# Kernel optimization log

Hardware: AMD Instinct MI355X
Metric: run time of the kernel (lower is better)

The kernel has to match this reference:

```python
import jax, jax.numpy as jnp
import numpy as np

N_NODES = 100000
N_EDGES = 1600000
EMB = 64       # embedding_dim
HID = 128      # hidden_channels
N_GRAPHS = 512
N_TASKS = 128
ATOM_VOCAB = 119
BOND_VOCAB = 16


def setup_inputs() -> dict:
    key = jax.random.key(0)
    ks = jax.random.split(key, 24)
    s = 0.02
    inp = {
        'x_idx': jax.random.randint(ks[0], (N_NODES,), 0, ATOM_VOCAB),
        'edge_index': jax.random.randint(ks[1], (2, N_EDGES), 0, N_NODES),
        'edge_attr_idx': jax.random.randint(ks[2], (N_EDGES,), 0, BOND_VOCAB),
        'batch': jnp.sort(jax.random.randint(ks[3], (N_NODES,), 0, N_GRAPHS)),
        'atom_emb': jax.random.normal(ks[4], (ATOM_VOCAB, EMB), jnp.float32) * s,
        'bond_emb': jax.random.normal(ks[5], (BOND_VOCAB, EMB), jnp.float32) * s,
        'w_edge0': jax.random.normal(ks[6], (EMB, EMB), jnp.float32) * s,
        'b_edge0': jnp.zeros((EMB,), jnp.float32),
        'w1_0': jax.random.normal(ks[7], (EMB, HID), jnp.float32) * s,
        'b1_0': jnp.zeros((HID,), jnp.float32),
        'w2_0': jax.random.normal(ks[8], (HID, HID), jnp.float32) * s,
        'b2_0': jnp.zeros((HID,), jnp.float32),
        'w_edge1': jax.random.normal(ks[9], (EMB, HID), jnp.float32) * s,
        'b_edge1': jnp.zeros((HID,), jnp.float32),
        'w1_1': jax.random.normal(ks[10], (HID, HID), jnp.float32) * s,
        'b1_1': jnp.zeros((HID,), jnp.float32),
        'w2_1': jax.random.normal(ks[11], (HID, HID), jnp.float32) * s,
        'b2_1': jnp.zeros((HID,), jnp.float32),
        'lin1_w': jax.random.normal(ks[12], (HID, HID), jnp.float32) * s,
        'lin1_b': jnp.zeros((HID,), jnp.float32),
        'lin2_w': jax.random.normal(ks[13], (HID, N_TASKS), jnp.float32) * s,
        'lin2_b': jnp.zeros((N_TASKS,), jnp.float32),
    }
    return inp


def _gine_conv(x, e, src, dst, we, be, w1, b1, w2, b2):
    # message: relu(x_j + Linear(edge_attr)); aggregate: scatter-add at dst
    msg = jax.nn.relu(x[src] + e @ we + be)            # [E, in_dim]
    agg = jax.ops.segment_sum(msg, dst, num_segments=N_NODES)
    h = x + agg                                        # (1+eps)*x with eps=0
    h = jax.nn.elu(h @ w1 + b1) @ w2 + b2              # GINE nn MLP
    return jax.nn.elu(h)                               # outer F.elu


def reference(x_idx, edge_index, edge_attr_idx, batch,
              atom_emb, bond_emb,
              w_edge0, b_edge0, w1_0, b1_0, w2_0, b2_0,
              w_edge1, b_edge1, w1_1, b1_1, w2_1, b2_1,
              lin1_w, lin1_b, lin2_w, lin2_b):
    x = atom_emb[x_idx]                                # [N, EMB]
    e = bond_emb[edge_attr_idx]                        # [E, EMB]
    src, dst = edge_index[0], edge_index[1]            # flow: source->target
    x = _gine_conv(x, e, src, dst, w_edge0, b_edge0, w1_0, b1_0, w2_0, b2_0)
    x = _gine_conv(x, e, src, dst, w_edge1, b_edge1, w1_1, b1_1, w2_1, b2_1)
    hg = jax.ops.segment_sum(x, batch, num_segments=N_GRAPHS)  # global_add_pool
    hg = jax.nn.relu(hg @ lin1_w + lin1_b)
    return hg @ lin2_w + lin2_b                        # [G, num_tasks]
```

## Files before the change

### kernel.cpp

```cpp
#include <hip/hip_runtime.h>
#include <hip/hip_bf16.h>

static const int NN = 100000;
static const int NE = 1600000;
static const int NG = 512;
static const int NB = 391;
static const int PS = 4608;
static const int CS = 4624;

typedef __attribute__((ext_vector_type(8))) short shortx8;
typedef __attribute__((ext_vector_type(4))) float floatx4;

__device__ __forceinline__ float bf2f(unsigned short u) {
  union { unsigned int i; float f; } v; v.i = ((unsigned int)u) << 16; return v.f;
}
__device__ __forceinline__ unsigned short f2bf(float f) {
  union { float f; unsigned int i; } v; v.f = f;
  return (unsigned short)((v.i + 0x7FFFu + ((v.i >> 16) & 1u)) >> 16);
}
__device__ __forceinline__ float elu_fast(float v) {
  return v > 0.f ? v : (__builtin_amdgcn_exp2f(v * 1.44269504f) - 1.f);
}

__global__ void k_prep(const float* __restrict__ bond,
                       const float* __restrict__ we0, const float* __restrict__ be0,
                       const float* __restrict__ we1, const float* __restrict__ be1,
                       const float* __restrict__ atom,
                       float* __restrict__ et1, float* __restrict__ M0,
                       float* __restrict__ hgf, int* __restrict__ bcursor,
                       const float* __restrict__ s0, const float* __restrict__ s1,
                       const float* __restrict__ s2, const float* __restrict__ s3,
                       const float* __restrict__ s4, const float* __restrict__ s5,
                       unsigned short* __restrict__ d0, unsigned short* __restrict__ d1,
                       unsigned short* __restrict__ d2, unsigned short* __restrict__ d3,
                       unsigned short* __restrict__ d4, unsigned short* __restrict__ d5) {
  int blk = blockIdx.x, t = threadIdx.x;
  if (blk < 8) {
    int i = blk * 256 + t;
    int b = i >> 7, c = i & 127;
    float acc = be1[c];
    for (int k = 0; k < 64; ++k) acc += bond[b * 64 + k] * we1[k * 128 + c];
    et1[i] = acc;
  } else if (blk < 484) {
    int i = (blk - 8) * 256 + t;
    int c = i & 63, b = (i >> 6) & 15, a = i >> 10;
    float acc = be0[c];
    for (int k = 0; k < 64; ++k) acc += bond[b * 64 + k] * we0[k * 64 + c];
    acc += atom[a * 64 + c];
    M0[i] = acc > 0.f ? acc : 0.f;
  } else if (blk < 868) {
    int task = (blk - 484) >> 6;
    int i = ((blk - 484) & 63) * 256 + t;
    const float* w; unsigned short* wz; int K;
    switch (task) {
      case 0: w = s0; wz = d0; K = 64; break;
      case 1: w = s1; wz = d1; K = 128; break;
      case 2: w = s2; wz = d2; K = 128; break;
      case 3: w = s3; wz = d3; K = 128; break;
      case 4: w = s4; wz = d4; K = 128; break;
      default: w = s5; wz = d5; K = 128; break;
    }
    if (i >= K * 128) return;
    int j = i & 7, lane = (i >> 3) & 63, ct = (i >> 9) & 7, s = i >> 12;
    int k = s * 32 + (lane >> 4) * 8 + j;
    int m = ct * 16 + (lane & 15);
    wz[i] = f2bf(w[k * 128 + m]);
  } else if (blk < 884) {
    int base = (blk - 868) * 4096;
#pragma unroll
    for (int k = 0; k < 16; ++k) hgf[base + k * 256 + t] = 0.f;
  } else {
    if (t < NB) bcursor[t] = t * PS;
    int u = t + 256;
    if (u < NB) bcursor[u] = u * PS;
  }
}

__global__ void k_bin(const int* __restrict__ src, const int* __restrict__ dstp,
                      const int* __restrict__ ea, const int* __restrict__ x_idx,
                      int* __restrict__ bcursor, uint2* __restrict__ pairs) {
  __shared__ int cnt[512];
  __shared__ int incl[512];
  __shared__ int cur[NB];
  __shared__ int rbase[NB];
  __shared__ uint2 stage[4096];
  int t = threadIdx.x;
  int e0 = blockIdx.x * 4096;
  int ecnt = NE - e0; if (ecnt > 4096) ecnt = 4096;
  cnt[t] = 0; cnt[t + 256] = 0;
  __syncthreads();
  for (int k = 0; k < 16; ++k) {
    int i = k * 256 + t;
    if (i < ecnt) atomicAdd(&cnt[dstp[e0 + i] >> 8], 1);
  }
  __syncthreads();
  incl[t] = cnt[t]; incl[t + 256] = cnt[t + 256];
  __syncthreads();
  for (int d = 1; d < 512; d <<= 1) {
    int v0 = (t >= d) ? incl[t - d] : 0;
    int v1 = (t + 256 >= d) ? incl[t + 256 - d] : 0;
    __syncthreads();
    incl[t] += v0; incl[t + 256] += v1;
    __syncthreads();
  }
  if (t < NB) { cur[t] = incl[t] - cnt[t]; if (cnt[t]) rbase[t] = atomicAdd(&bcursor[t], cnt[t]); }
  int u = t + 256;
  if (u < NB) { cur[u] = incl[u] - cnt[u]; if (cnt[u]) rbase[u] = atomicAdd(&bcursor[u], cnt[u]); }
  __syncthreads();
  for (int k = 0; k < 16; ++k) {
    int i = k * 256 + t;
    if (i < ecnt) {
      int e = e0 + i;
      int d = dstp[e];
      int s = src[e];
      unsigned int pk = (unsigned int)s | ((unsigned int)(x_idx[s] * 16 + ea[e]) << 17);
      int p = atomicAdd(&cur[d >> 8], 1);
      stage[p] = make_uint2((unsigned int)d, pk);
    }
  }
  __syncthreads();
  for (int j = t; j < ecnt; j += 256) {
    uint2 p = stage[j];
    int b = (int)(p.x >> 8);
    int excl = incl[b] - cnt[b];
    pairs[rbase[b] + (j - excl)] = p;
  }
}

__global__ void k_fine(const uint2* __restrict__ pairs, const int* __restrict__ bcursor,
                       int* __restrict__ offs, int* __restrict__ cnts,
                       unsigned int* __restrict__ csr0, unsigned int* __restrict__ csr1) {
  __shared__ int cnt[256];
  __shared__ int incl[256];
  __shared__ int cur[256];
  int b = blockIdx.x;
  int t = threadIdx.x;
  int start = b * PS;
  int endv = bcursor[b];
  int cbase = b * CS;
  int base_n = b << 8;
  cnt[t] = 0;
  __syncthreads();
  for (int j = start + t; j < endv; j += 256)
    atomicAdd(&cnt[(int)pairs[j].x - base_n], 1);
  __syncthreads();
  incl[t] = cnt[t];
  __syncthreads();
  for (int d = 1; d < 256; d <<= 1) {
    int v = (t >= d) ? incl[t - d] : 0;
    __syncthreads();
    incl[t] += v;
    __syncthreads();
  }
  int excl = incl[t] - cnt[t];
  cur[t] = excl;
  int node = base_n + t;
  if (node < NN) { offs[node] = cbase + excl; cnts[node] = cnt[t]; }
  __syncthreads();
  for (int j = start + t; j < endv; j += 256) {
    uint2 p = pairs[j];
    int pos = cbase + atomicAdd(&cur[(int)p.x - base_n], 1);
    unsigned int pk = p.y;
    unsigned int idx17 = pk >> 17;
    csr0[pos] = idx17 << 8;
    csr1[pos] = ((pk & 0x1FFFFu) << 8) | (idx17 & 15u);
  }
  __syncthreads();
  int total = incl[255];
  if (t < 16) { csr0[cbase + total + t] = 0u; csr1[cbase + total + t] = 0u; }
}

__global__ __launch_bounds__(256) void k_agg0(
    const int* __restrict__ x_idx, const float* __restrict__ atom,
    const float* __restrict__ M0, const int* __restrict__ offs,
    const int* __restrict__ cnts,
    const unsigned int* __restrict__ csr0, unsigned short* __restrict__ h0) {
  int t = threadIdx.x, lane = t & 63;
  int n = __builtin_amdgcn_readfirstlane(blockIdx.x * 4 + (t >> 6));
  if (n >= NN) return;
  int s = offs[n], e = s + cnts[n];
  const char* Mb = (const char*)M0;
  unsigned int voff = (unsigned int)lane * 4u;
  float acc = *(const float*)((const char*)atom + ((size_t)(unsigned)x_idx[n] << 8) + voff);
  for (int i = s; i < e; i += 8) {
    unsigned int q0 = csr0[i + 0], q1 = csr0[i + 1], q2 = csr0[i + 2], q3 = csr0[i + 3];
    unsigned int q4 = csr0[i + 4], q5 = csr0[i + 5], q6 = csr0[i + 6], q7 = csr0[i + 7];
    float m1 = (i + 1 < e) ? 1.f : 0.f, m2 = (i + 2 < e) ? 1.f : 0.f;
    float m3 = (i + 3 < e) ? 1.f : 0.f, m4 = (i + 4 < e) ? 1.f : 0.f;
    float m5 = (i + 5 < e) ? 1.f : 0.f, m6 = (i + 6 < e) ? 1.f : 0.f;
    float m7 = (i + 7 < e) ? 1.f : 0.f;
    float v0 = *(const float*)(Mb + q0 + voff);
    float v1 = *(const float*)(Mb + q1 + voff);
    float v2 = *(const float*)(Mb + q2 + voff);
    float v3 = *(const float*)(Mb + q3 + voff);
    float v4 = *(const float*)(Mb + q4 + voff);
    float v5 = *(const float*)(Mb + q5 + voff);
    float v6 = *(const float*)(Mb + q6 + voff);
    float v7 = *(const float*)(Mb + q7 + voff);
    acc += v0;
    acc = fmaf(m1, v1, acc); acc = fmaf(m2, v2, acc);
    acc = fmaf(m3, v3, acc); acc = fmaf(m4, v4, acc);
    acc = fmaf(m5, v5, acc); acc = fmaf(m6, v6, acc);
    acc = fmaf(m7, v7, acc);
  }
  h0[(size_t)n * 64 + lane] = f2bf(acc);
}

__global__ __launch_bounds__(256) void k_agg1(
    const unsigned short* __restrict__ x1, const float* __restrict__ et1,
    const int* __restrict__ offs, const int* __restrict__ cnts,
    const unsigned int* __restrict__ csr1, unsigned short* __restrict__ h1) {
  __shared__ float etl[2048];
  int t = threadIdx.x;
#pragma unroll
  for (int k = 0; k < 8; ++k) etl[k * 256 + t] = et1[k * 256 + t];
  __syncthreads();
  int lane = t & 63;
  int n = __builtin_amdgcn_readfirstlane(blockIdx.x * 4 + (t >> 6));
  if (n >= NN) return;
  int s = offs[n], e = s + cnts[n];
  const char* xb = (const char*)x1;
  unsigned int voff = (unsigned int)lane * 4u;
  const char* etb = (const char*)etl + (size_t)lane * 8u;
  unsigned int xv = *(const unsigned int*)(xb + ((size_t)(unsigned)n << 8) + voff);
  float ax = bf2f((unsigned short)(xv & 0xFFFF));
  float ay = bf2f((unsigned short)(xv >> 16));
  for (int i = s; i < e; i += 8) {
    unsigned int q0 = csr1[i + 0], q1 = csr1[i + 1], q2 = csr1[i + 2], q3 = csr1[i + 3];
    unsigned int q4 = csr1[i + 4], q5 = csr1[i + 5], q6 = csr1[i + 6], q7 = csr1[i + 7];
    float m1 = (i + 1 < e) ? 1.f : 0.f, m2 = (i + 2 < e) ? 1.f : 0.f;
    float m3 = (i + 3 < e) ? 1.f : 0.f, m4 = (i + 4 < e) ? 1.f : 0.f;
    float m5 = (i + 5 < e) ? 1.f : 0.f, m6 = (i + 6 < e) ? 1.f : 0.f;
    float m7 = (i + 7 < e) ? 1.f : 0.f;
    unsigned int v0 = *(const unsigned int*)(xb + (q0 & 0xFFFFFF00u) + voff);
    unsigned int v1 = *(const unsigned int*)(xb + (q1 & 0xFFFFFF00u) + voff);
    unsigned int v2 = *(const unsigned int*)(xb + (q2 & 0xFFFFFF00u) + voff);
    unsigned int v3 = *(const unsigned int*)(xb + (q3 & 0xFFFFFF00u) + voff);
    unsigned int v4 = *(const unsigned int*)(xb + (q4 & 0xFFFFFF00u) + voff);
    unsigned int v5 = *(const unsigned int*)(xb + (q5 & 0xFFFFFF00u) + voff);
    unsigned int v6 = *(const unsigned int*)(xb + (q6 & 0xFFFFFF00u) + voff);
    unsigned int v7 = *(const unsigned int*)(xb + (q7 & 0xFFFFFF00u) + voff);
    float2 e0 = *(const float2*)(etb + ((q0 & 15u) << 9));
    float2 e1 = *(const float2*)(etb + ((q1 & 15u) << 9));
    float2 e2 = *(const float2*)(etb + ((q2 & 15u) << 9));
    float2 e3 = *(const float2*)(etb + ((q3 & 15u) << 9));
    float2 e4 = *(const float2*)(etb + ((q4 & 15u) << 9));
    float2 e5 = *(const float2*)(etb + ((q5 & 15u) << 9));
    float2 e6 = *(const float2*)(etb + ((q6 & 15u) << 9));
    float2 e7 = *(const float2*)(etb + ((q7 & 15u) << 9));
    float mx, my;
    mx = bf2f((unsigned short)(v0 & 0xFFFF)) + e0.x; my = bf2f((unsigned short)(v0 >> 16)) + e0.y;
    ax += fmaxf(mx, 0.f); ay += fmaxf(my, 0.f);
    mx = bf2f((unsigned short)(v1 & 0xFFFF)) + e1.x; my = bf2f((unsigned short)(v1 >> 16)) + e1.y;
    ax = fmaf(m1, fmaxf(mx, 0.f), ax); ay = fmaf(m1, fmaxf(my, 0.f), ay);
    mx = bf2f((unsigned short)(v2 & 0xFFFF)) + e2.x; my = bf2f((unsigned short)(v2 >> 16)) + e2.y;
    ax = fmaf(m2, fmaxf(mx, 0.f), ax); ay = fmaf(m2, fmaxf(my, 0.f), ay);
    mx = bf2f((unsigned short)(v3 & 0xFFFF)) + e3.x; my = bf2f((unsigned short)(v3 >> 16)) + e3.y;
    ax = fmaf(m3, fmaxf(mx, 0.f), ax); ay = fmaf(m3, fmaxf(my, 0.f), ay);
    mx = bf2f((unsigned short)(v4 & 0xFFFF)) + e4.x; my = bf2f((unsigned short)(v4 >> 16)) + e4.y;
    ax = fmaf(m4, fmaxf(mx, 0.f), ax); ay = fmaf(m4, fmaxf(my, 0.f), ay);
    mx = bf2f((unsigned short)(v5 & 0xFFFF)) + e5.x; my = bf2f((unsigned short)(v5 >> 16)) + e5.y;
    ax = fmaf(m5, fmaxf(mx, 0.f), ax); ay = fmaf(m5, fmaxf(my, 0.f), ay);
    mx = bf2f((unsigned short)(v6 & 0xFFFF)) + e6.x; my = bf2f((unsigned short)(v6 >> 16)) + e6.y;
    ax = fmaf(m6, fmaxf(mx, 0.f), ax); ay = fmaf(m6, fmaxf(my, 0.f), ay);
    mx = bf2f((unsigned short)(v7 & 0xFFFF)) + e7.x; my = bf2f((unsigned short)(v7 >> 16)) + e7.y;
    ax = fmaf(m7, fmaxf(mx, 0.f), ax); ay = fmaf(m7, fmaxf(my, 0.f), ay);
  }
  unsigned int o = (unsigned int)f2bf(ax) | ((unsigned int)f2bf(ay) << 16);
  *(unsigned int*)(h1 + (size_t)n * 128 + lane * 2) = o;
}

template <int K1>
__global__ __launch_bounds__(256) void k_mlp_t(
    const unsigned short* __restrict__ in,
    const unsigned short* __restrict__ w1z, const float* __restrict__ b1,
    const unsigned short* __restrict__ w2z, const float* __restrict__ b2,
    unsigned short* __restrict__ outb, int N) {
  __shared__ unsigned short tls[4][16][136];
  __shared__ unsigned short b2s[16384];
  int t = threadIdx.x;
  int lane = t & 63;
  int wave = t >> 6;
  int rlo = lane & 15, quad = lane >> 4;

#pragma unroll
  for (int k = 0; k < 8; ++k)
    *(shortx8*)&b2s[(k * 256 + t) * 8] = *(const shortx8*)&w2z[(k * 256 + t) * 8];

  float bm1[8], bm2[8];
#pragma unroll
  for (int ct = 0; ct < 8; ++ct) { bm1[ct] = b1[ct * 16 + rlo]; bm2[ct] = b2[ct * 16 + rlo]; }

  __syncthreads();

#pragma unroll
  for (int t2 = 0; t2 < 2; ++t2) {
    int row0 = blockIdx.x * 128 + t2 * 64 + wave * 16;
    int arow = row0 + rlo;

    floatx4 acc[8];
#pragma unroll
    for (int ct = 0; ct < 8; ++ct) { acc[ct][0]=0.f; acc[ct][1]=0.f; acc[ct][2]=0.f; acc[ct][3]=0.f; }
    const int NS = K1 >> 5;
#pragma unroll
    for (int s = 0; s < NS; ++s) {
      shortx8 a = {0,0,0,0,0,0,0,0};
      if (arow < N) a = *(const shortx8*)(in + (size_t)arow * K1 + s * 32 + quad * 8);
      const unsigned short* wp = w1z + ((size_t)(s * 8) * 64 + lane) * 8;
#pragma unroll
      for (int ct = 0; ct < 8; ++ct) {
        shortx8 b = *(const shortx8*)(wp + ct * 512);
        acc[ct] = __builtin_amdgcn_mfma_f32_16x16x32_bf16(a, b, acc[ct], 0, 0, 0);
      }
    }
#pragma unroll
    for (int ct = 0; ct < 8; ++ct) {
#pragma unroll
      for (int r = 0; r < 4; ++r) {
        float v = elu_fast(acc[ct][r] + bm1[ct]);
        tls[wave][quad * 4 + r][ct * 16 + rlo] = f2bf(v);
      }
    }

    floatx4 acc2[8];
#pragma unroll
    for (int ct = 0; ct < 8; ++ct) { acc2[ct][0]=0.f; acc2[ct][1]=0.f; acc2[ct][2]=0.f; acc2[ct][3]=0.f; }
#pragma unroll
    for (int s = 0; s < 4; ++s) {
      shortx8 a = *(const shortx8*)&tls[wave][rlo][s * 32 + quad * 8];
      const unsigned short* wp = &b2s[((s * 8) * 64 + lane) * 8];
#pragma unroll
      for (int ct = 0; ct < 8; ++ct) {
        shortx8 b = *(const shortx8*)(wp + ct * 512);
        acc2[ct] = __builtin_amdgcn_mfma_f32_16x16x32_bf16(a, b, acc2[ct], 0, 0, 0);
      }
    }
#pragma unroll
    for (int ct = 0; ct < 8; ++ct) {
#pragma unroll
      for (int r = 0; r < 4; ++r) {
        float v = elu_fast(acc2[ct][r] + bm2[ct]);
        tls[wave][quad * 4 + r][ct * 16 + rlo] = f2bf(v);
      }
    }
    int srow = lane >> 2;
    int schunk = lane & 3;
    int grow = row0 + srow;
#pragma unroll
    for (int k = 0; k < 4; ++k) {
      int ch = schunk + k * 4;
      if (grow < N)
        *(shortx8*)(outb + (size_t)grow * 128 + ch * 8) =
            *(const shortx8*)&tls[wave][srow][ch * 8];
    }
  }
}

__global__ __launch_bounds__(256) void k_pool(
    const unsigned short* __restrict__ x2, const int* __restrict__ batch,
    float* __restrict__ hgf) {
  int gt = blockIdx.x * 256 + threadIdx.x;
  int chunk = gt >> 6, lane = gt & 63;
  int n0 = chunk * 32;
  if (n0 >= NN) return;
  int nend = n0 + 32; if (nend > NN) nend = NN;
  float ax = 0.f, ay = 0.f;
  const unsigned short* xp = x2 + lane * 2;
  int gcur = batch[n0];
  for (int n = n0; n < nend; ++n) {
    int g = batch[n];
    if (g != gcur) {
      atomicAdd(&hgf[gcur * 128 + lane * 2], ax);
      atomicAdd(&hgf[gcur * 128 + lane * 2 + 1], ay);
      ax = 0.f; ay = 0.f; gcur = g;
    }
    unsigned int v = *(const unsigned int*)(xp + (size_t)n * 128);
    ax += bf2f((unsigned short)(v & 0xFFFF));
    ay += bf2f((unsigned short)(v >> 16));
  }
  atomicAdd(&hgf[gcur * 128 + lane * 2], ax);
  atomicAdd(&hgf[gcur * 128 + lane * 2 + 1], ay);
}

__global__ void k_head(const float* __restrict__ in,
                       const unsigned short* __restrict__ w1z, const float* __restrict__ b1,
                       const unsigned short* __restrict__ w2z, const float* __restrict__ b2,
                       float* __restrict__ outf, int N) {
  __shared__ unsigned short tls[4][16][136];
  int lane = threadIdx.x & 63;
  int wave = threadIdx.x >> 6;
  int row0 = blockIdx.x * 64 + wave * 16;
  int rlo = lane & 15, quad = lane >> 4;
  int arow = row0 + rlo;
  floatx4 acc[8];
#pragma unroll
  for (int ct = 0; ct < 8; ++ct) { acc[ct][0]=0.f; acc[ct][1]=0.f; acc[ct][2]=0.f; acc[ct][3]=0.f; }
#pragma unroll
  for (int s = 0; s < 4; ++s) {
    shortx8 a = {0,0,0,0,0,0,0,0};
    if (arow < N) {
      const float* rp = in + (size_t)arow * 128 + s * 32 + quad * 8;
      float4 f0 = *(const float4*)rp;
      float4 f1 = *(const float4*)(rp + 4);
      a[0] = (short)f2bf(f0.x); a[1] = (short)f2bf(f0.y);
      a[2] = (short)f2bf(f0.z); a[3] = (short)f2bf(f0.w);
      a[4] = (short)f2bf(f1.x); a[5] = (short)f2bf(f1.y);
      a[6] = (short)f2bf(f1.z); a[7] = (short)f2bf(f1.w);
    }
    const unsigned short* wp = w1z + ((size_t)(s * 8) * 64 + lane) * 8;
#pragma unroll
    for (int ct = 0; ct < 8; ++ct) {
      shortx8 b = *(const shortx8*)(wp + ct * 512);
      acc[ct] = __builtin_amdgcn_mfma_f32_16x16x32_bf16(a, b, acc[ct], 0, 0, 0);
    }
  }
#pragma unroll
  for (int ct = 0; ct < 8; ++ct) {
    float bm = b1[ct * 16 + rlo];
#pragma unroll
    for (int r = 0; r < 4; ++r) {
      float v = acc[ct][r] + bm;
      v = v > 0.f ? v : 0.f;
      tls[wave][quad * 4 + r][ct * 16 + rlo] = f2bf(v);
    }
  }
  __syncthreads();
  floatx4 acc2[8];
#pragma unroll
  for (int ct = 0; ct < 8; ++ct) { acc2[ct][0]=0.f; acc2[ct][1]=0.f; acc2[ct][2]=0.f; acc2[ct][3]=0.f; }
#pragma unroll
  for (int s = 0; s < 4; ++s) {
    shortx8 a = *(const shortx8*)&tls[wave][rlo][s * 32 + quad * 8];
    const unsigned short* wp = w2z + ((size_t)(s * 8) * 64 + lane) * 8;
#pragma unroll
    for (int ct = 0; ct < 8; ++ct) {
      shortx8 b = *(const shortx8*)(wp + ct * 512);
      acc2[ct] = __builtin_amdgcn_mfma_f32_16x16x32_bf16(a, b, acc2[ct], 0, 0, 0);
    }
  }
#pragma unroll
  for (int ct = 0; ct < 8; ++ct) {
    float bm = b2[ct * 16 + rlo];
#pragma unroll
    for (int r = 0; r < 4; ++r) {
      int rr = row0 + quad * 4 + r;
      if (rr < N) outf[(size_t)rr * 128 + ct * 16 + rlo] = acc2[ct][r] + bm;
    }
  }
}

extern "C" void kernel_launch(void* const* d_in, const int* in_sizes, int n_in,
                              void* d_out, int out_size, void* d_ws, size_t ws_size,
                              hipStream_t stream) {
  const int* x_idx  = (const int*)d_in[0];
  const int* e_src  = (const int*)d_in[1];
  const int* e_dst  = e_src + NE;
  const int* e_attr = (const int*)d_in[2];
  const int* batch  = (const int*)d_in[3];
  const float* atom = (const float*)d_in[4];
  const float* bond = (const float*)d_in[5];
  const float* we0  = (const float*)d_in[6];
  const float* be0  = (const float*)d_in[7];
  const float* w1_0 = (const float*)d_in[8];
  const float* b1_0 = (const float*)d_in[9];
  const float* w2_0 = (const float*)d_in[10];
  const float* b2_0 = (const float*)d_in[11];
  const float* we1  = (const float*)d_in[12];
  const float* be1  = (const float*)d_in[13];
  const float* w1_1 = (const float*)d_in[14];
  const float* b1_1 = (const float*)d_in[15];
  const float* w2_1 = (const float*)d_in[16];
  const float* b2_1 = (const float*)d_in[17];
  const float* l1w  = (const float*)d_in[18];
  const float* l1b  = (const float*)d_in[19];
  const float* l2w  = (const float*)d_in[20];
  const float* l2b  = (const float*)d_in[21];

  char* ws = (char*)d_ws;
  size_t off = 0;
  auto alloc = [&](size_t bytes) -> void* {
    void* p = ws + off;
    off = (off + bytes + 255) & ~(size_t)255;
    return p;
  };
  int* bcursor = (int*)alloc((size_t)NB * 4);
  int* offs    = (int*)alloc((size_t)NN * 4);
  int* cnts    = (int*)alloc((size_t)NN * 4);
  float* et1   = (float*)alloc(16 * 128 * 4);
  float* M0    = (float*)alloc((size_t)1904 * 64 * 4);
  float* hgf   = (float*)alloc((size_t)NG * 128 * 4);
  unsigned short* w1_0z = (unsigned short*)alloc(64 * 128 * 2);
  unsigned short* w2_0z = (unsigned short*)alloc(128 * 128 * 2);
  unsigned short* w1_1z = (unsigned short*)alloc(128 * 128 * 2);
  unsigned short* w2_1z = (unsigned short*)alloc(128 * 128 * 2);
  unsigned short* l1z   = (unsigned short*)alloc(128 * 128 * 2);
  unsigned short* l2z   = (unsigned short*)alloc(128 * 128 * 2);
  uint2* pairs = (uint2*)alloc((size_t)NB * PS * 8);
  unsigned int* csr0 = (unsigned int*)alloc((size_t)NB * CS * 4);
  unsigned int* csr1 = (unsigned int*)alloc((size_t)NB * CS * 4);
  unsigned short* x1 = (unsigned short*)alloc((size_t)NN * 128 * 2);
  unsigned short* h1 = (unsigned short*)alloc((size_t)NN * 128 * 2);
  unsigned short* h0 = (unsigned short*)pairs;
  unsigned short* x2 = h1;

  k_prep<<<885, 256, 0, stream>>>(bond, we0, be0, we1, be1, atom, et1, M0, hgf, bcursor,
                                  w1_0, w2_0, w1_1, w2_1, l1w, l2w,
                                  w1_0z, w2_0z, w1_1z, w2_1z, l1z, l2z);
  k_bin<<<(NE + 4095) / 4096, 256, 0, stream>>>(e_src, e_dst, e_attr, x_idx, bcursor, pairs);
  k_fine<<<NB, 256, 0, stream>>>(pairs, bcursor, offs, cnts, csr0, csr1);
  k_agg0<<<NN / 4, 256, 0, stream>>>(x_idx, atom, M0, offs, cnts, csr0, h0);
  k_mlp_t<64><<<(NN + 127) / 128, 256, 0, stream>>>(h0, w1_0z, b1_0, w2_0z, b2_0, x1, NN);
  k_agg1<<<NN / 4, 256, 0, stream>>>(x1, et1, offs, cnts, csr1, h1);
  k_mlp_t<128><<<(NN + 127) / 128, 256, 0, stream>>>(h1, w1_1z, b1_1, w2_1z, b2_1, x2, NN);
  k_pool<<<(((NN + 31) / 32) * 64 + 255) / 256, 256, 0, stream>>>(x2, batch, hgf);
  k_head<<<(NG + 63) / 64, 256, 0, stream>>>(hgf, l1z, l1b, l2z, l2b, (float*)d_out, NG);
}
```

Measured before the change: 329.5 us.

## Store edge-message table in bf16 and split wavefront halves across edges in agg0

The precomputed relu(atom+bond) message table M0 is now stored as bf16 instead of fp32, which halves its footprint and the bytes gathered per edge. In k_agg0 each wavefront splits into two 32-lane halves that process alternate edges, each lane accumulating two channels from a packed 32-bit load. The halves are combined with a cross-lane shuffle before the write. This cuts per-edge gather traffic and doubles edge parallelism per wave, at the cost of bf16 rounding in the message table and extra select and unpack instructions.

Measured after the change: 325.9 us. No clear change (-1.1%).

```diff
diff --git a/kernel.cpp b/kernel.cpp
--- a/kernel.cpp
+++ b/kernel.cpp
@@ -26,7 +26,7 @@
                        const float* __restrict__ we0, const float* __restrict__ be0,
                        const float* __restrict__ we1, const float* __restrict__ be1,
                        const float* __restrict__ atom,
-                       float* __restrict__ et1, float* __restrict__ M0,
+                       float* __restrict__ et1, unsigned short* __restrict__ M0,
                        float* __restrict__ hgf, int* __restrict__ bcursor,
                        const float* __restrict__ s0, const float* __restrict__ s1,
                        const float* __restrict__ s2, const float* __restrict__ s3,
@@ -47,7 +47,7 @@
     float acc = be0[c];
     for (int k = 0; k < 64; ++k) acc += bond[b * 64 + k] * we0[k * 64 + c];
     acc += atom[a * 64 + c];
-    M0[i] = acc > 0.f ? acc : 0.f;
+    M0[i] = f2bf(acc > 0.f ? acc : 0.f);
   } else if (blk < 868) {
     int task = (blk - 484) >> 6;
     int i = ((blk - 484) & 63) * 256 + t;
@@ -162,7 +162,7 @@
     int pos = cbase + atomicAdd(&cur[(int)p.x - base_n], 1);
     unsigned int pk = p.y;
     unsigned int idx17 = pk >> 17;
-    csr0[pos] = idx17 << 8;
+    csr0[pos] = idx17 << 7;
     csr1[pos] = ((pk & 0x1FFFFu) << 8) | (idx17 & 15u);
   }
   __syncthreads();
@@ -172,38 +172,75 @@
 
 __global__ __launch_bounds__(256) void k_agg0(
     const int* __restrict__ x_idx, const float* __restrict__ atom,
-    const float* __restrict__ M0, const int* __restrict__ offs,
+    const unsigned short* __restrict__ M0, const int* __restrict__ offs,
     const int* __restrict__ cnts,
     const unsigned int* __restrict__ csr0, unsigned short* __restrict__ h0) {
   int t = threadIdx.x, lane = t & 63;
+  int half = lane >> 5, c = lane & 31;
   int n = __builtin_amdgcn_readfirstlane(blockIdx.x * 4 + (t >> 6));
   if (n >= NN) return;
   int s = offs[n], e = s + cnts[n];
   const char* Mb = (const char*)M0;
-  unsigned int voff = (unsigned int)lane * 4u;
-  float acc = *(const float*)((const char*)atom + ((size_t)(unsigned)x_idx[n] << 8) + voff);
-  for (int i = s; i < e; i += 8) {
-    unsigned int q0 = csr0[i + 0], q1 = csr0[i + 1], q2 = csr0[i + 2], q3 = csr0[i + 3];
-    unsigned int q4 = csr0[i + 4], q5 = csr0[i + 5], q6 = csr0[i + 6], q7 = csr0[i + 7];
-    float m1 = (i + 1 < e) ? 1.f : 0.f, m2 = (i + 2 < e) ? 1.f : 0.f;
-    float m3 = (i + 3 < e) ? 1.f : 0.f, m4 = (i + 4 < e) ? 1.f : 0.f;
-    float m5 = (i + 5 < e) ? 1.f : 0.f, m6 = (i + 6 < e) ? 1.f : 0.f;
-    float m7 = (i + 7 < e) ? 1.f : 0.f;
-    float v0 = *(const float*)(Mb + q0 + voff);
-    float v1 = *(const float*)(Mb + q1 + voff);
-    float v2 = *(const float*)(Mb + q2 + voff);
-    float v3 = *(const float*)(Mb + q3 + voff);
-    float v4 = *(const float*)(Mb + q4 + voff);
-    float v5 = *(const float*)(Mb + q5 + voff);
-    float v6 = *(const float*)(Mb + q6 + voff);
-    float v7 = *(const float*)(Mb + q7 + voff);
-    acc += v0;
-    acc = fmaf(m1, v1, acc); acc = fmaf(m2, v2, acc);
-    acc = fmaf(m3, v3, acc); acc = fmaf(m4, v4, acc);
-    acc = fmaf(m5, v5, acc); acc = fmaf(m6, v6, acc);
-    acc = fmaf(m7, v7, acc);
-  }
-  h0[(size_t)n * 64 + lane] = f2bf(acc);
+  unsigned int voff = (unsigned int)c * 4u;
+  float ax = 0.f, ay = 0.f;
+  if (half == 0) {
+    float2 sv = *(const float2*)((const char*)atom +
+                                 ((size_t)(unsigned)x_idx[n] << 8) + (size_t)c * 8u);
+    ax = sv.x; ay = sv.y;
+  }
+  float fh = (float)half;
+  for (int i = s; i < e; i += 16) {
+    unsigned int a0 = csr0[i + 0],  b0 = csr0[i + 1];
+    unsigned int a1 = csr0[i + 2],  b1 = csr0[i + 3];
+    unsigned int a2 = csr0[i + 4],  b2 = csr0[i + 5];
+    unsigned int a3 = csr0[i + 6],  b3 = csr0[i + 7];
+    unsigned int a4 = csr0[i + 8],  b4 = csr0[i + 9];
+    unsigned int a5 = csr0[i + 10], b5 = csr0[i + 11];
+    unsigned int a6 = csr0[i + 12], b6 = csr0[i + 13];
+    unsigned int a7 = csr0[i + 14], b7 = csr0[i + 15];
+    unsigned int q0 = half ? b0 : a0, q1 = half ? b1 : a1;
+    unsigned int q2 = half ? b2 : a2, q3 = half ? b3 : a3;
+    unsigned int q4 = half ? b4 : a4, q5 = half ? b5 : a5;
+    unsigned int q6 = half ? b6 : a6, q7 = half ? b7 : a7;
+    float m0 = (i + 0 + half < e) ? 1.f : 0.f;
+    float m1 = (i + 2 + half < e) ? 1.f : 0.f;
+    float m2 = (i + 4 + half < e) ? 1.f : 0.f;
+    float m3 = (i + 6 + half < e) ? 1.f : 0.f;
+    float m4 = (i + 8 + half < e) ? 1.f : 0.f;
+    float m5 = (i + 10 + half < e) ? 1.f : 0.f;
+    float m6 = (i + 12 + half < e) ? 1.f : 0.f;
+    float m7 = (i + 14 + half < e) ? 1.f : 0.f;
+    unsigned int v0 = *(const unsigned int*)(Mb + q0 + voff);
+    unsigned int v1 = *(const unsigned int*)(Mb + q1 + voff);
+    unsigned int v2 = *(const unsigned int*)(Mb + q2 + voff);
+    unsigned int v3 = *(const unsigned int*)(Mb + q3 + voff);
+    unsigned int v4 = *(const unsigned int*)(Mb + q4 + voff);
+    unsigned int v5 = *(const unsigned int*)(Mb + q5 + voff);
+    unsigned int v6 = *(const unsigned int*)(Mb + q6 + voff);
+    unsigned int v7 = *(const unsigned int*)(Mb + q7 + voff);
+    ax = fmaf(m0, bf2f((unsigned short)(v0 & 0xFFFF)), ax);
+    ay = fmaf(m0, bf2f((unsigned short)(v0 >> 16)), ay);
+    ax = fmaf(m1, bf2f((unsigned short)(v1 & 0xFFFF)), ax);
+    ay = fmaf(m1, bf2f((unsigned short)(v1 >> 16)), ay);
+    ax = fmaf(m2, bf2f((unsigned short)(v2 & 0xFFFF)), ax);
+    ay = fmaf(m2, bf2f((unsigned short)(v2 >> 16)), ay);
+    ax = fmaf(m3, bf2f((unsigned short)(v3 & 0xFFFF)), ax);
+    ay = fmaf(m3, bf2f((unsigned short)(v3 >> 16)), ay);
+    ax = fmaf(m4, bf2f((unsigned short)(v4 & 0xFFFF)), ax);
+    ay = fmaf(m4, bf2f((unsigned short)(v4 >> 16)), ay);
+    ax = fmaf(m5, bf2f((unsigned short)(v5 & 0xFFFF)), ax);
+    ay = fmaf(m5, bf2f((unsigned short)(v5 >> 16)), ay);
+    ax = fmaf(m6, bf2f((unsigned short)(v6 & 0xFFFF)), ax);
+    ay = fmaf(m6, bf2f((unsigned short)(v6 >> 16)), ay);
+    ax = fmaf(m7, bf2f((unsigned short)(v7 & 0xFFFF)), ax);
+    ay = fmaf(m7, bf2f((unsigned short)(v7 >> 16)), ay);
+  }
+  ax += __shfl_xor(ax, 32);
+  ay += __shfl_xor(ay, 32);
+  if (half == 0) {
+    unsigned int o = (unsigned int)f2bf(ax) | ((unsigned int)f2bf(ay) << 16);
+    *(unsigned int*)(h0 + (size_t)n * 64 + c * 2) = o;
+  }
 }
 
 __global__ __launch_bounds__(256) void k_agg1(
@@ -487,7 +524,7 @@
   int* offs    = (int*)alloc((size_t)NN * 4);
   int* cnts    = (int*)alloc((size_t)NN * 4);
   float* et1   = (float*)alloc(16 * 128 * 4);
-  float* M0    = (float*)alloc((size_t)1904 * 64 * 4);
+  unsigned short* M0 = (unsigned short*)alloc((size_t)1904 * 64 * 2);
   float* hgf   = (float*)alloc((size_t)NG * 128 * 4);
   unsigned short* w1_0z = (unsigned short*)alloc(64 * 128 * 2);
   unsigned short* w2_0z = (unsigned short*)alloc(128 * 128 * 2);
```
